# Performance work log

Hardware: AMD Instinct MI355X
Metric: run time of the kernel (lower is better)

Reference implementation:

```python
import jax, jax.numpy as jnp
import numpy as np

MODEL_DIM = 1024
NUM_HEADS = 16
K_DIM = MODEL_DIM // NUM_HEADS


def setup_inputs() -> dict:
    key = jax.random.key(0)
    kx, kw1, kw2 = jax.random.split(key, 3)
    B, L, D = 4, 2048, MODEL_DIM
    x = jax.random.normal(kx, (B, L, D), dtype=jnp.float32)
    # nn.Linear(D, 3D, bias=False): y = x @ W^T; store transposed form [D, 3D]
    scale1 = 1.0 / np.sqrt(D)
    Wqkv = jax.random.uniform(kw1, (D, 3 * D), dtype=jnp.float32, minval=-scale1, maxval=scale1)
    Wout = jax.random.uniform(kw2, (D, D), dtype=jnp.float32, minval=-scale1, maxval=scale1)
    return {"x": x, "Wqkv": Wqkv, "Wout": Wout}


def reference(x, Wqkv, Wout):
    B, L, D = x.shape
    H, Kd = NUM_HEADS, K_DIM
    qkv = x @ Wqkv  # [B, L, 3D]
    q, k, v = jnp.split(qkv, 3, axis=-1)

    def heads(t):  # [B, L, D] -> [B, H, L, Kd]
        return t.reshape(B, L, H, Kd).transpose(0, 2, 1, 3)

    qh, kh, vh = heads(q), heads(k), heads(v)
    scores = jnp.einsum('bhqd,bhkd->bhqk', qh, kh) / jnp.sqrt(jnp.float32(Kd))
    causal = jnp.triu(jnp.ones((L, L), dtype=bool), k=1)  # True above diagonal
    scores = jnp.where(causal, -jnp.inf, scores)
    probs = jax.nn.softmax(scores, axis=-1)
    attended = jnp.einsum('bhqk,bhkd->bhqd', probs, vh)
    concatted = attended.transpose(0, 2, 1, 3).reshape(B, L, D)
    # dropout is identity in eval mode
    return concatted @ Wout
```

## Files before the change

### kernel.cpp

```cpp
#include <hip/hip_runtime.h>

typedef unsigned short u16;
typedef unsigned int   u32;
typedef __bf16   bf16x8 __attribute__((ext_vector_type(8)));
typedef float    f32x4  __attribute__((ext_vector_type(4)));
typedef u16      u16x4  __attribute__((ext_vector_type(4)));
typedef u16      u16x8  __attribute__((ext_vector_type(8)));
typedef u32      u32x2  __attribute__((ext_vector_type(2)));
typedef u32      u32x4  __attribute__((ext_vector_type(4)));

#if __has_builtin(__builtin_amdgcn_exp2f)
#define EXP2(x) __builtin_amdgcn_exp2f(x)
#else
#define EXP2(x) exp2f(x)
#endif

__device__ __forceinline__ u16 f2bf(float f) {
    unsigned u = __float_as_uint(f);
    u += 0x7FFFu + ((u >> 16) & 1u);
    return (u16)(u >> 16);
}

__device__ __forceinline__ u32 pack_bf16(float a, float b) {
#if __has_builtin(__builtin_amdgcn_cvt_pk_bf16_f32)
    typedef __bf16 bf16x2 __attribute__((ext_vector_type(2)));
    bf16x2 r = __builtin_amdgcn_cvt_pk_bf16_f32(a, b);
    return __builtin_bit_cast(u32, r);
#else
    return (u32)f2bf(a) | ((u32)f2bf(b) << 16);
#endif
}

__device__ __forceinline__ void async_copy16(const u16* g, u16* l) {
    __builtin_amdgcn_global_load_lds(
        (const __attribute__((address_space(1))) unsigned*)g,
        (__attribute__((address_space(3))) unsigned*)l, 16, 0, 0);
}

__device__ __forceinline__ bf16x8 lds_frag(const u16* p) {
    return *(const bf16x8*)p;
}

__global__ __launch_bounds__(256) void prep(const float* __restrict__ x,
                                            const float* __restrict__ Wqkv,
                                            const float* __restrict__ Wout,
                                            u16* __restrict__ xb,
                                            u16* __restrict__ wqkv_t,
                                            u16* __restrict__ wout_t) {
    __shared__ u16 t[64 * 72];
    const int bid = blockIdx.x;
    const int tid = threadIdx.x;

    if (bid >= 1024) {
        size_t i = ((size_t)(bid - 1024) * 256 + tid) * 8;
        float4 v0 = *(const float4*)(x + i);
        float4 v1 = *(const float4*)(x + i + 4);
        u16x8 o = { f2bf(v0.x), f2bf(v0.y), f2bf(v0.z), f2bf(v0.w),
                    f2bf(v1.x), f2bf(v1.y), f2bf(v1.z), f2bf(v1.w) };
        *(u16x8*)(xb + i) = o;
        return;
    }

    const float* W;  u16* Wt;  int Kd, Nd, n0, k0;
    if (bid < 768) { W = Wqkv; Wt = wqkv_t; Kd = 1024; Nd = 3072;
                     n0 = (bid % 48) * 64; k0 = (bid / 48) * 64; }
    else           { W = Wout; Wt = wout_t; Kd = 1024; Nd = 1024;
                     n0 = ((bid - 768) % 16) * 64; k0 = ((bid - 768) / 16) * 64; }
#pragma unroll
    for (int i = 0; i < 4; ++i) {
        int lin = i * 256 + tid;
        int kr = lin >> 4, nc = (lin & 15) << 2;
        float4 v = *(const float4*)(W + (size_t)(k0 + kr) * Nd + n0 + nc);
        u16x4 o = { f2bf(v.x), f2bf(v.y), f2bf(v.z), f2bf(v.w) };
        *(u16x4*)&t[kr * 72 + nc] = o;
    }
    __syncthreads();
#pragma unroll
    for (int i = 0; i < 2; ++i) {
        int lin = i * 256 + tid;
        int nr = lin >> 3, kc = (lin & 7) << 3;
        u16x8 o;
#pragma unroll
        for (int jj = 0; jj < 8; ++jj) o[jj] = t[(kc + jj) * 72 + nr];
        *(u16x8*)(Wt + (size_t)(n0 + nr) * Kd + k0 + kc) = o;
    }
}

__global__ __launch_bounds__(256) void gemm_qkv(const u16* __restrict__ A,
                                                const u16* __restrict__ Bt,
                                                u16* __restrict__ outb,
                                                int K, int N) {
    __shared__ u16 As[2][128 * 32];
    __shared__ u16 Bs[2][128 * 32];
    const int tid = threadIdx.x;
    const int lane = tid & 63;
    const int wv = tid >> 6;
    const int wr = (wv >> 1) * 64;
    const int wc = (wv & 1) * 64;
    const int qd = lane >> 4;
    const int c  = lane & 15;
    const int m0 = blockIdx.y * 128;
    const int n0 = blockIdx.x * 128;

    const int srow = tid >> 2;
    const int sg = ((tid & 3) ^ ((srow >> 1) & 3)) << 3;

    const u16* Ag0 = A  + (size_t)(m0 +      srow) * K + sg;
    const u16* Ag1 = A  + (size_t)(m0 + 64 + srow) * K + sg;
    const u16* Bg0 = Bt + (size_t)(n0 +      srow) * K + sg;
    const u16* Bg1 = Bt + (size_t)(n0 + 64 + srow) * K + sg;

    const u32 fsw = (qd ^ ((c >> 1) & 3)) << 3;
    const u32 a_off = (wr + c) * 32 + fsw;
    const u32 b_off = (wc + c) * 32 + fsw;

    f32x4 acc[4][4] = {};

    async_copy16(Ag0, &As[0][tid * 8]);
    async_copy16(Ag1, &As[0][2048 + tid * 8]);
    async_copy16(Bg0, &Bs[0][tid * 8]);
    async_copy16(Bg1, &Bs[0][2048 + tid * 8]);

    int p = 0;
    for (int k0 = 0; k0 < K; k0 += 32) {
        __syncthreads();
        if (k0 + 32 < K) {
            const int np = p ^ 1;
            async_copy16(Ag0 + k0 + 32, &As[np][tid * 8]);
            async_copy16(Ag1 + k0 + 32, &As[np][2048 + tid * 8]);
            async_copy16(Bg0 + k0 + 32, &Bs[np][tid * 8]);
            async_copy16(Bg1 + k0 + 32, &Bs[np][2048 + tid * 8]);
        }
        bf16x8 af[4], bfr[4];
#pragma unroll
        for (int i = 0; i < 4; ++i) af[i]  = lds_frag(&As[p][a_off + i * 512]);
#pragma unroll
        for (int j = 0; j < 4; ++j) bfr[j] = lds_frag(&Bs[p][b_off + j * 512]);
#pragma unroll
        for (int i = 0; i < 4; ++i)
#pragma unroll
            for (int j = 0; j < 4; ++j)
                acc[i][j] = __builtin_amdgcn_mfma_f32_16x16x32_bf16(af[i], bfr[j], acc[i][j], 0, 0, 0);
        p ^= 1;
    }

#pragma unroll
    for (int i = 0; i < 4; ++i)
#pragma unroll
        for (int j = 0; j < 4; ++j) {
            int n = n0 + wc + j * 16 + c;
            int which = n >> 10, h = (n >> 6) & 15, kd = n & 63;
            int m_base = m0 + wr + i * 16 + qd * 4;
            int b = m_base >> 11, l0 = m_base & 2047;
            int bh = b * 16 + h;
            if (which == 2) {
                u32x2 o2;
                o2[0] = pack_bf16(acc[i][j][0], acc[i][j][1]);
                o2[1] = pack_bf16(acc[i][j][2], acc[i][j][3]);
                *(u32x2*)(outb + (size_t)(128 + bh) * 131072 + (size_t)kd * 2048 + l0) = o2;
            } else if (which == 0) {
#pragma unroll
                for (int r = 0; r < 4; ++r)
                    outb[(size_t)bh * 131072 + (size_t)(l0 + r) * 64 + kd] =
                        f2bf(acc[i][j][r] * 0.1803368801f);
            } else {
#pragma unroll
                for (int r = 0; r < 4; ++r)
                    outb[(size_t)(64 + bh) * 131072 + (size_t)(l0 + r) * 64 + kd] =
                        f2bf(acc[i][j][r]);
            }
        }
}

__global__ __launch_bounds__(256) void gemm_out(const u16* __restrict__ A,
                                                const u16* __restrict__ Bt,
                                                float* __restrict__ outf,
                                                int K, int N) {
    __shared__ u16 As[2][64 * 32];
    __shared__ u16 Bs[2][128 * 32];
    const int tid = threadIdx.x;
    const int lane = tid & 63;
    const int wv = tid >> 6;
    const int wr = (wv >> 1) * 32;
    const int wc = (wv & 1) * 64;
    const int qd = lane >> 4;
    const int c  = lane & 15;
    const int m0 = blockIdx.y * 64;
    const int n0 = blockIdx.x * 128;

    const int srow = tid >> 2;
    const int sg = ((tid & 3) ^ ((srow >> 1) & 3)) << 3;

    const u16* Ag0 = A  + (size_t)(m0 +      srow) * K + sg;
    const u16* Bg0 = Bt + (size_t)(n0 +      srow) * K + sg;
    const u16* Bg1 = Bt + (size_t)(n0 + 64 + srow) * K + sg;

    const u32 fsw = (qd ^ ((c >> 1) & 3)) << 3;
    const u32 a_off = (wr + c) * 32 + fsw;
    const u32 b_off = (wc + c) * 32 + fsw;

    f32x4 acc[2][4] = {};

    async_copy16(Ag0, &As[0][tid * 8]);
    async_copy16(Bg0, &Bs[0][tid * 8]);
    async_copy16(Bg1, &Bs[0][2048 + tid * 8]);

    int p = 0;
    for (int k0 = 0; k0 < K; k0 += 32) {
        __syncthreads();
        if (k0 + 32 < K) {
            const int np = p ^ 1;
            async_copy16(Ag0 + k0 + 32, &As[np][tid * 8]);
            async_copy16(Bg0 + k0 + 32, &Bs[np][tid * 8]);
            async_copy16(Bg1 + k0 + 32, &Bs[np][2048 + tid * 8]);
        }
        bf16x8 af[2], bfr[4];
#pragma unroll
        for (int i = 0; i < 2; ++i) af[i]  = lds_frag(&As[p][a_off + i * 512]);
#pragma unroll
        for (int j = 0; j < 4; ++j) bfr[j] = lds_frag(&Bs[p][b_off + j * 512]);
#pragma unroll
        for (int i = 0; i < 2; ++i)
#pragma unroll
            for (int j = 0; j < 4; ++j)
                acc[i][j] = __builtin_amdgcn_mfma_f32_16x16x32_bf16(af[i], bfr[j], acc[i][j], 0, 0, 0);
        p ^= 1;
    }

#pragma unroll
    for (int i = 0; i < 2; ++i)
#pragma unroll
        for (int j = 0; j < 4; ++j)
#pragma unroll
            for (int r = 0; r < 4; ++r) {
                int m = m0 + wr + i * 16 + qd * 4 + r;
                int n = n0 + wc + j * 16 + c;
                outf[(size_t)m * N + n] = acc[i][j][r];
            }
}

__global__ __launch_bounds__(256, 2) void attn_kernel(const u16* __restrict__ qkv,
                                                      u16* __restrict__ att) {
    __shared__ u16 Ks[2][128 * 64];
    __shared__ u16 Vt[2][64 * 128];
    __shared__ u16 Ps[4][16 * 128];

    const int tid = threadIdx.x;
    const int lane = tid & 63;
    const int w = tid >> 6;
    const int qd = lane >> 4;
    const int c = lane & 15;

    const int flat = blockIdx.x + 8 * blockIdx.y;
    const int bh = (flat & 7) + 8 * ((flat >> 3) & 7);
    const int bx = flat >> 6;
    const int b = bh >> 4, h = bh & 15;

    const u16* Qg = qkv + (size_t)bh * 131072;
    const u16* Kg = qkv + (size_t)(64 + bh) * 131072;
    const u16* Vg = qkv + (size_t)(128 + bh) * 131072;

    u32 k_go[4], v_go[4], s_lo[4];
#pragma unroll
    for (int it = 0; it < 4; ++it) {
        int lin = it * 256 + tid;
        int krw = lin >> 3, kch = lin & 7;
        k_go[it] = krw * 64 + ((kch ^ (krw & 7)) << 3);
        int vrw = lin >> 4, vch = lin & 15;
        v_go[it] = vrw * 2048 + ((vch ^ (vrw & 15)) << 3);
        s_lo[it] = lin * 8;
    }

    u32 kf_off[2];
#pragma unroll
    for (int ks = 0; ks < 2; ++ks)
        kf_off[ks] = c * 64 + (((ks * 4 + qd) ^ (c & 7)) << 3);
    u32 vf_off[4];
#pragma unroll
    for (int kc = 0; kc < 4; ++kc)
        vf_off[kc] = c * 128 + (((kc * 4 + qd) ^ c) << 3);
    u16* psw = &Ps[w][c * 128 + (qd & 1) * 4];
    const u16* psr = &Ps[w][c * 128];

#pragma unroll
    for (int seg = 0; seg < 2; ++seg) {
        const int qt = seg ? (15 - bx) : bx;
        const int qa_row = qt * 128 + w * 32 + c;
        const int qb_row = qa_row + 16;

        bf16x8 qa[2], qb[2];
#pragma unroll
        for (int ks = 0; ks < 2; ++ks) {
            qa[ks] = *(const bf16x8*)(Qg + (size_t)qa_row * 64 + ks * 32 + qd * 8);
            qb[ks] = *(const bf16x8*)(Qg + (size_t)qb_row * 64 + ks * 32 + qd * 8);
        }

        f32x4 acca[4] = {}, accb[4] = {};
        float ra = 0.0f, rb = 0.0f;

        const int nkt = qt + 1;
        int p = 0;
        for (int kt = 0; kt < nkt; ++kt) {
            __syncthreads();
            if (kt == 0) {
#pragma unroll
                for (int it = 0; it < 4; ++it) {
                    async_copy16(Kg + (size_t)kt * 8192 + k_go[it], &Ks[0][s_lo[it]]);
                    async_copy16(Vg + (size_t)kt * 128  + v_go[it], &Vt[0][s_lo[it]]);
                }
                __syncthreads();
            }
            if (kt + 1 < nkt) {
                const int nt = kt + 1, np = p ^ 1;
#pragma unroll
                for (int it = 0; it < 4; ++it) {
                    async_copy16(Kg + (size_t)nt * 8192 + k_go[it], &Ks[np][s_lo[it]]);
                    async_copy16(Vg + (size_t)nt * 128  + v_go[it], &Vt[np][s_lo[it]]);
                }
            }

            const u16* ksb = Ks[p];
            const u16* vtb = Vt[p];

            f32x4 sa[8] = {}, sb[8] = {};
#pragma unroll
            for (int ks = 0; ks < 2; ++ks) {
                const u16* kp = ksb + kf_off[ks];
#pragma unroll
                for (int f = 0; f < 8; ++f) {
                    bf16x8 kf = lds_frag(kp + f * 1024);
                    sa[f] = __builtin_amdgcn_mfma_f32_16x16x32_bf16(kf, qa[ks], sa[f], 0, 0, 0);
                    sb[f] = __builtin_amdgcn_mfma_f32_16x16x32_bf16(kf, qb[ks], sb[f], 0, 0, 0);
                }
            }

            if (kt == qt) {
#pragma unroll
                for (int f = 0; f < 8; ++f)
#pragma unroll
                    for (int r = 0; r < 4; ++r) {
                        int key = kt * 128 + f * 16 + qd * 4 + r;
                        if (key > qa_row) sa[f][r] = -3e38f;
                        if (key > qb_row) sb[f][r] = -3e38f;
                    }
            }

#pragma unroll
            for (int f = 0; f < 8; ++f)
#pragma unroll
                for (int r = 0; r < 4; ++r) {
                    float pa = EXP2(sa[f][r] - 8.0f);
                    float pb = EXP2(sb[f][r] - 8.0f);
                    sa[f][r] = pa; sb[f][r] = pb;
                    ra += pa; rb += pb;
                }

            u32x4 pfa[4], pfb[4];
#pragma unroll
            for (int f = 0; f < 8; ++f) {
                u32x2 pw;
                pw[0] = pack_bf16(sa[f][0], sa[f][1]);
                pw[1] = pack_bf16(sa[f][2], sa[f][3]);
                *(u32x2*)(psw + (((f * 2 + (qd >> 1)) ^ c) << 3)) = pw;
            }
#pragma unroll
            for (int kc = 0; kc < 4; ++kc)
                pfa[kc] = *(const u32x4*)(psr + (((kc * 4 + qd) ^ c) << 3));
#pragma unroll
            for (int f = 0; f < 8; ++f) {
                u32x2 pw;
                pw[0] = pack_bf16(sb[f][0], sb[f][1]);
                pw[1] = pack_bf16(sb[f][2], sb[f][3]);
                *(u32x2*)(psw + (((f * 2 + (qd >> 1)) ^ c) << 3)) = pw;
            }
#pragma unroll
            for (int kc = 0; kc < 4; ++kc)
                pfb[kc] = *(const u32x4*)(psr + (((kc * 4 + qd) ^ c) << 3));

#pragma unroll
            for (int kc = 0; kc < 4; ++kc) {
                const u16* vp = vtb + vf_off[kc];
                bf16x8 pa = __builtin_bit_cast(bf16x8, pfa[kc]);
                bf16x8 pb = __builtin_bit_cast(bf16x8, pfb[kc]);
#pragma unroll
                for (int jo = 0; jo < 4; ++jo) {
                    bf16x8 vf = lds_frag(vp + jo * 2048);
                    acca[jo] = __builtin_amdgcn_mfma_f32_16x16x32_bf16(vf, pa, acca[jo], 0, 0, 0);
                    accb[jo] = __builtin_amdgcn_mfma_f32_16x16x32_bf16(vf, pb, accb[jo], 0, 0, 0);
                }
            }
            p ^= 1;
        }

        ra += __shfl_xor(ra, 16, 64);
        ra += __shfl_xor(ra, 32, 64);
        rb += __shfl_xor(rb, 16, 64);
        rb += __shfl_xor(rb, 32, 64);
        float ia = __builtin_amdgcn_rcpf(ra), ib = __builtin_amdgcn_rcpf(rb);
        u16* ar = att + ((size_t)b * 2048 + qa_row) * 1024 + h * 64;
        u16* br = att + ((size_t)b * 2048 + qb_row) * 1024 + h * 64;
#pragma unroll
        for (int jo = 0; jo < 4; ++jo) {
            u32x2 oa, ob;
            oa[0] = pack_bf16(acca[jo][0] * ia, acca[jo][1] * ia);
            oa[1] = pack_bf16(acca[jo][2] * ia, acca[jo][3] * ia);
            ob[0] = pack_bf16(accb[jo][0] * ib, accb[jo][1] * ib);
            ob[1] = pack_bf16(accb[jo][2] * ib, accb[jo][3] * ib);
            *(u32x2*)(ar + jo * 16 + qd * 4) = oa;
            *(u32x2*)(br + jo * 16 + qd * 4) = ob;
        }
    }
}

extern "C" void kernel_launch(void* const* d_in, const int* in_sizes, int n_in,
                              void* d_out, int out_size, void* d_ws, size_t ws_size,
                              hipStream_t stream) {
    const float* x    = (const float*)d_in[0];
    const float* Wqkv = (const float*)d_in[1];
    const float* Wout = (const float*)d_in[2];
    float* out = (float*)d_out;

    char* ws = (char*)d_ws;
    u16* x_bf   = (u16*)(ws);
    u16* wqkv_t = (u16*)(ws + 16777216);
    u16* wout_t = (u16*)(ws + 23068672);
    u16* qkv_h  = (u16*)(ws + 25165824);
    u16* att    = (u16*)(ws + 75497472);

    prep<<<dim3(5120), dim3(256), 0, stream>>>(x, Wqkv, Wout, x_bf, wqkv_t, wout_t);
    gemm_qkv<<<dim3(24, 64), dim3(256), 0, stream>>>(x_bf, wqkv_t, qkv_h, 1024, 3072);
    attn_kernel<<<dim3(8, 64), dim3(256), 0, stream>>>(qkv_h, att);
    gemm_out<<<dim3(8, 128), dim3(256), 0, stream>>>(att, wout_t, out, 1024, 1024);
}
```

Measured before the change: 248.2 us.

## Load GEMM B fragments directly to registers and swizzle block order

Both GEMM kernels stop staging the weight operand in shared memory. Each lane now loads its B fragments from global memory into registers, prefetched one k-step ahead, which removes LDS writes, reads and footprint for B. Block indices are remapped into 8x8 groups to improve L2 reuse, and K/N become compile-time constants. The attention softmax also drops its fixed -8 exponent offset. The risks are less coalesced global B loads and possible overflow for large scores.

```diff
diff --git a/kernel.cpp b/kernel.cpp
--- a/kernel.cpp
+++ b/kernel.cpp
@@ -88,10 +88,9 @@
 
 __global__ __launch_bounds__(256) void gemm_qkv(const u16* __restrict__ A,
                                                 const u16* __restrict__ Bt,
-                                                u16* __restrict__ outb,
-                                                int K, int N) {
+                                                u16* __restrict__ outb) {
+    const int K = 1024;
     __shared__ u16 As[2][128 * 32];
-    __shared__ u16 Bs[2][128 * 32];
     const int tid = threadIdx.x;
     const int lane = tid & 63;
     const int wv = tid >> 6;
@@ -99,27 +98,35 @@
     const int wc = (wv & 1) * 64;
     const int qd = lane >> 4;
     const int c  = lane & 15;
-    const int m0 = blockIdx.y * 128;
-    const int n0 = blockIdx.x * 128;
+
+    const int flat = blockIdx.x;
+    const int s = flat >> 6, t = flat & 63;
+    const int bx = (t & 7) + 8 * (s % 3);
+    const int by = (t >> 3) + 8 * (s / 3);
+    const int m0 = by * 128;
+    const int n0 = bx * 128;
 
     const int srow = tid >> 2;
     const int sg = ((tid & 3) ^ ((srow >> 1) & 3)) << 3;
 
-    const u16* Ag0 = A  + (size_t)(m0 +      srow) * K + sg;
-    const u16* Ag1 = A  + (size_t)(m0 + 64 + srow) * K + sg;
-    const u16* Bg0 = Bt + (size_t)(n0 +      srow) * K + sg;
-    const u16* Bg1 = Bt + (size_t)(n0 + 64 + srow) * K + sg;
+    const u16* Ag0 = A + (size_t)(m0 +      srow) * K + sg;
+    const u16* Ag1 = A + (size_t)(m0 + 64 + srow) * K + sg;
 
     const u32 fsw = (qd ^ ((c >> 1) & 3)) << 3;
     const u32 a_off = (wr + c) * 32 + fsw;
-    const u32 b_off = (wc + c) * 32 + fsw;
+
+    const u16* bg[4];
+#pragma unroll
+    for (int j = 0; j < 4; ++j)
+        bg[j] = Bt + (size_t)(n0 + wc + j * 16 + c) * K + qd * 8;
 
     f32x4 acc[4][4] = {};
 
     async_copy16(Ag0, &As[0][tid * 8]);
     async_copy16(Ag1, &As[0][2048 + tid * 8]);
-    async_copy16(Bg0, &Bs[0][tid * 8]);
-    async_copy16(Bg1, &Bs[0][2048 + tid * 8]);
+    bf16x8 bcur[4], bnxt[4];
+#pragma unroll
+    for (int j = 0; j < 4; ++j) bcur[j] = *(const bf16x8*)(bg[j]);
 
     int p = 0;
     for (int k0 = 0; k0 < K; k0 += 32) {
@@ -128,19 +135,19 @@
             const int np = p ^ 1;
             async_copy16(Ag0 + k0 + 32, &As[np][tid * 8]);
             async_copy16(Ag1 + k0 + 32, &As[np][2048 + tid * 8]);
-            async_copy16(Bg0 + k0 + 32, &Bs[np][tid * 8]);
-            async_copy16(Bg1 + k0 + 32, &Bs[np][2048 + tid * 8]);
-        }
-        bf16x8 af[4], bfr[4];
-#pragma unroll
-        for (int i = 0; i < 4; ++i) af[i]  = lds_frag(&As[p][a_off + i * 512]);
-#pragma unroll
-        for (int j = 0; j < 4; ++j) bfr[j] = lds_frag(&Bs[p][b_off + j * 512]);
+#pragma unroll
+            for (int j = 0; j < 4; ++j) bnxt[j] = *(const bf16x8*)(bg[j] + k0 + 32);
+        }
+        bf16x8 af[4];
+#pragma unroll
+        for (int i = 0; i < 4; ++i) af[i] = lds_frag(&As[p][a_off + i * 512]);
 #pragma unroll
         for (int i = 0; i < 4; ++i)
 #pragma unroll
             for (int j = 0; j < 4; ++j)
-                acc[i][j] = __builtin_amdgcn_mfma_f32_16x16x32_bf16(af[i], bfr[j], acc[i][j], 0, 0, 0);
+                acc[i][j] = __builtin_amdgcn_mfma_f32_16x16x32_bf16(af[i], bcur[j], acc[i][j], 0, 0, 0);
+#pragma unroll
+        for (int j = 0; j < 4; ++j) bcur[j] = bnxt[j];
         p ^= 1;
     }
 
@@ -174,10 +181,9 @@
 
 __global__ __launch_bounds__(256) void gemm_out(const u16* __restrict__ A,
                                                 const u16* __restrict__ Bt,
-                                                float* __restrict__ outf,
-                                                int K, int N) {
+                                                float* __restrict__ outf) {
+    const int K = 1024, N = 1024;
     __shared__ u16 As[2][64 * 32];
-    __shared__ u16 Bs[2][128 * 32];
     const int tid = threadIdx.x;
     const int lane = tid & 63;
     const int wv = tid >> 6;
@@ -185,25 +191,33 @@
     const int wc = (wv & 1) * 64;
     const int qd = lane >> 4;
     const int c  = lane & 15;
-    const int m0 = blockIdx.y * 64;
-    const int n0 = blockIdx.x * 128;
+
+    const int flat = blockIdx.x;
+    const int s = flat >> 6, t = flat & 63;
+    const int bx = t & 7;
+    const int by = (t >> 3) + 8 * s;
+    const int m0 = by * 64;
+    const int n0 = bx * 128;
 
     const int srow = tid >> 2;
     const int sg = ((tid & 3) ^ ((srow >> 1) & 3)) << 3;
 
-    const u16* Ag0 = A  + (size_t)(m0 +      srow) * K + sg;
-    const u16* Bg0 = Bt + (size_t)(n0 +      srow) * K + sg;
-    const u16* Bg1 = Bt + (size_t)(n0 + 64 + srow) * K + sg;
+    const u16* Ag0 = A + (size_t)(m0 + srow) * K + sg;
 
     const u32 fsw = (qd ^ ((c >> 1) & 3)) << 3;
     const u32 a_off = (wr + c) * 32 + fsw;
-    const u32 b_off = (wc + c) * 32 + fsw;
+
+    const u16* bg[4];
+#pragma unroll
+    for (int j = 0; j < 4; ++j)
+        bg[j] = Bt + (size_t)(n0 + wc + j * 16 + c) * K + qd * 8;
 
     f32x4 acc[2][4] = {};
 
     async_copy16(Ag0, &As[0][tid * 8]);
-    async_copy16(Bg0, &Bs[0][tid * 8]);
-    async_copy16(Bg1, &Bs[0][2048 + tid * 8]);
+    bf16x8 bcur[4], bnxt[4];
+#pragma unroll
+    for (int j = 0; j < 4; ++j) bcur[j] = *(const bf16x8*)(bg[j]);
 
     int p = 0;
     for (int k0 = 0; k0 < K; k0 += 32) {
@@ -211,19 +225,19 @@
         if (k0 + 32 < K) {
             const int np = p ^ 1;
             async_copy16(Ag0 + k0 + 32, &As[np][tid * 8]);
-            async_copy16(Bg0 + k0 + 32, &Bs[np][tid * 8]);
-            async_copy16(Bg1 + k0 + 32, &Bs[np][2048 + tid * 8]);
-        }
-        bf16x8 af[2], bfr[4];
-#pragma unroll
-        for (int i = 0; i < 2; ++i) af[i]  = lds_frag(&As[p][a_off + i * 512]);
-#pragma unroll
-        for (int j = 0; j < 4; ++j) bfr[j] = lds_frag(&Bs[p][b_off + j * 512]);
+#pragma unroll
+            for (int j = 0; j < 4; ++j) bnxt[j] = *(const bf16x8*)(bg[j] + k0 + 32);
+        }
+        bf16x8 af[2];
+#pragma unroll
+        for (int i = 0; i < 2; ++i) af[i] = lds_frag(&As[p][a_off + i * 512]);
 #pragma unroll
         for (int i = 0; i < 2; ++i)
 #pragma unroll
             for (int j = 0; j < 4; ++j)
-                acc[i][j] = __builtin_amdgcn_mfma_f32_16x16x32_bf16(af[i], bfr[j], acc[i][j], 0, 0, 0);
+                acc[i][j] = __builtin_amdgcn_mfma_f32_16x16x32_bf16(af[i], bcur[j], acc[i][j], 0, 0, 0);
+#pragma unroll
+        for (int j = 0; j < 4; ++j) bcur[j] = bnxt[j];
         p ^= 1;
     }
 
@@ -349,8 +363,8 @@
             for (int f = 0; f < 8; ++f)
 #pragma unroll
                 for (int r = 0; r < 4; ++r) {
-                    float pa = EXP2(sa[f][r] - 8.0f);
-                    float pb = EXP2(sb[f][r] - 8.0f);
+                    float pa = EXP2(sa[f][r]);
+                    float pb = EXP2(sb[f][r]);
                     sa[f][r] = pa; sb[f][r] = pb;
                     ra += pa; rb += pb;
                 }
@@ -428,7 +442,7 @@
     u16* att    = (u16*)(ws + 75497472);
 
     prep<<<dim3(5120), dim3(256), 0, stream>>>(x, Wqkv, Wout, x_bf, wqkv_t, wout_t);
-    gemm_qkv<<<dim3(24, 64), dim3(256), 0, stream>>>(x_bf, wqkv_t, qkv_h, 1024, 3072);
+    gemm_qkv<<<dim3(1536), dim3(256), 0, stream>>>(x_bf, wqkv_t, qkv_h);
     attn_kernel<<<dim3(8, 64), dim3(256), 0, stream>>>(qkv_h, att);
-    gemm_out<<<dim3(8, 128), dim3(256), 0, stream>>>(att, wout_t, out, 1024, 1024);
-}
+    gemm_out<<<dim3(1024), dim3(256), 0, stream>>>(att, wout_t, out);
+}
```

Result: slower. 339.1 us (+36.6%).
